# Optimization experiments

Hardware: AMD Instinct MI355X
Metric: run time of the kernel (lower is better)

The kernel has to match this reference:

```python
import jax, jax.numpy as jnp
import numpy as np

BATCH = 16384
N_IN = 128
N_FEAT = N_IN + N_IN * (N_IN + 1) // 2  # 8384
N_OUT = 512


def setup_inputs() -> dict:
    key = jax.random.key(0)
    k1, k2 = jax.random.split(key)
    x = jax.random.normal(k1, (BATCH, N_IN), dtype=jnp.float32)
    # xavier_uniform_ on (in_features, out_features)
    limit = float(np.sqrt(6.0 / (N_FEAT + N_OUT)))
    weight = jax.random.uniform(k2, (N_FEAT, N_OUT), dtype=jnp.float32, minval=-limit, maxval=limit)
    bias = jnp.zeros((N_OUT,), dtype=jnp.float32)
    return {"x": x, "weight": weight, "bias": bias}


def _quadratic_expand(x):
    # Upper-triangle (i<=j) pairwise products in row-major order,
    # matching the torch nested loop (ih, ih+jh).
    n = x.shape[1]
    iu, ju = jnp.triu_indices(n)
    cross = x[:, iu] * x[:, ju]  # [B, n(n+1)/2]
    return jnp.concatenate([x, cross], axis=1)  # [B, n + n(n+1)/2]


def reference(x, weight, bias):
    xc = _quadratic_expand(x)
    return jnp.matmul(xc, weight) + bias
```

## Files before the change

kernel.cpp:

```cpp
#include <hip/hip_runtime.h>

#define NIN    128
#define NOUT   512
#define NBATCH 16384
#define KF     8384
#define KP2    8832
#define NG     (KP2 / 8)
#define NTK2   (KP2 / 64)
#define XSP    136
#define NTK    (KF / 64)
#define XP     136
#define AP     72

typedef float f32x4 __attribute__((ext_vector_type(4)));
typedef _Float16 f16x8 __attribute__((ext_vector_type(8)));
typedef _Float16 f16x4 __attribute__((ext_vector_type(4)));
typedef __bf16 bf16x8 __attribute__((ext_vector_type(8)));
typedef unsigned int u32x4 __attribute__((ext_vector_type(4)));

__device__ __forceinline__ int triS(int i) { return (i * (257 - i)) >> 1; }

__global__ void k_tbl(unsigned int* __restrict__ tbl)
{
  int g = blockIdx.x * 256 + threadIdx.x;
  if (g >= NG) return;
  unsigned int e;
  if (g < 16) {
    e = 135u | ((unsigned)(g * 8) << 16);
  } else {
    int gp = g - 16;
    int b = 0;
    #pragma unroll
    for (int bb = 1; bb <= 15; ++bb) {
      int C = 8 * (16 * bb - bb * (bb - 1) / 2);
      if (gp >= C) b = bb;
    }
    int C   = 8 * (16 * b - b * (b - 1) / 2);
    int r   = gp - C;
    int per = 16 - b;
    int i   = 8 * b + r / per;
    int q   = r % per;
    e = (unsigned)i | ((unsigned)(8 * b + 8 * q) << 16);
  }
  tbl[g] = e;
}

__global__ void k_wt2(const float* __restrict__ W,
                      const unsigned int* __restrict__ tbl,
                      _Float16* __restrict__ Wt)
{
  __shared__ _Float16 tile[64][65];
  const int kb   = blockIdx.x >> 3;
  const int nbw  = blockIdx.x & 7;
  const int lane = threadIdx.x & 63;
  const int grp  = threadIdx.x >> 6;
  #pragma unroll 4
  for (int it = 0; it < 16; ++it) {
    int kl = it * 4 + grp;
    int kp = kb * 64 + kl;
    unsigned int e = tbl[kp >> 3];
    int i = (int)(e & 0xFFFFu);
    int j = (int)(e >> 16) + (kp & 7);
    float v = 0.f;
    if (i == 135) {
      v = W[(size_t)kp * NOUT + nbw * 64 + lane];
    } else if (j >= i) {
      int src = 128 + i * 128 - i * (i - 1) / 2 + (j - i);
      v = W[(size_t)src * NOUT + nbw * 64 + lane];
    }
    tile[kl][lane] = (_Float16)v;
  }
  __syncthreads();
  #pragma unroll 4
  for (int it = 0; it < 16; ++it) {
    int nl = it * 4 + grp;
    Wt[(size_t)(nbw * 64 + nl) * KP2 + kb * 64 + lane] = tile[lane][nl];
  }
}

__global__ __launch_bounds__(256, 2) void k_gemm8(
    const float* __restrict__ X,
    const _Float16* __restrict__ Wt,
    const float* __restrict__ bias,
    const unsigned int* __restrict__ tbl,
    float* __restrict__ out)
{
  __shared__ __align__(16) _Float16 xS[128 * XSP];
  __shared__ __align__(16) _Float16 Bt[2][128 * 64];
  __shared__ unsigned short tbl_s[NG];

  const int tid  = threadIdx.x;
  const int lane = tid & 63;
  const int wid  = tid >> 6;
  const int wm   = wid & 1;
  const int wk   = wid >> 1;
  const int mb   = blockIdx.x >> 2;
  const int nb   = blockIdx.x & 3;

  for (int g = tid; g < NG; g += 256) {
    unsigned int e = tbl[g];
    tbl_s[g] = (unsigned short)((e & 0xFFu) | ((e >> 16) << 8));
  }

  {
    const float* xg = X + (size_t)mb * 128 * NIN;
    const int m = tid >> 1, h = tid & 1;
    #pragma unroll
    for (int it = 0; it < 16; ++it) {
      int c4 = h * 64 + it * 4;
      f32x4 v = *reinterpret_cast<const f32x4*>(xg + m * NIN + c4);
      f16x4 b;
      #pragma unroll
      for (int e2 = 0; e2 < 4; ++e2) b[e2] = (_Float16)v[e2];
      *reinterpret_cast<f16x4*>(&xS[m * XSP + c4]) = b;
    }
    if (tid < 128) xS[tid * XSP + 135] = (_Float16)1.0f;
  }

  const int sn = tid >> 3;
  const int sc = tid & 7;
  const _Float16* wrow = Wt + (size_t)(nb * 128 + sn) * KP2 + sc * 8;
  f16x8 pf[8];

  f32x4 acc[4][8];
  #pragma unroll
  for (int a = 0; a < 4; ++a)
    #pragma unroll
    for (int b = 0; b < 8; ++b)
      acc[a][b] = f32x4{0.f, 0.f, 0.f, 0.f};

  #pragma unroll
  for (int r = 0; r < 8; ++r) {
    int t = r >> 2, rep = r & 3;
    pf[r] = *reinterpret_cast<const f16x8*>(wrow + (size_t)rep * 32 * KP2 + t * 64);
  }
  #pragma unroll
  for (int r = 0; r < 8; ++r) {
    int t = r >> 2, rep = r & 3;
    int n = sn + rep * 32;
    *reinterpret_cast<f16x8*>(&Bt[t][n * 64 + ((sc ^ (n & 7)) * 8)]) = pf[r];
  }
  __syncthreads();

  const int NP = NTK2 / 2;
  for (int p = 0; p < NP; ++p) {
    const int kt = 2 * p + wk;
    if (p + 1 < NP) {
      #pragma unroll
      for (int r = 0; r < 8; ++r) {
        int t = r >> 2, rep = r & 3;
        pf[r] = *reinterpret_cast<const f16x8*>(
            wrow + (size_t)rep * 32 * KP2 + (size_t)(2 * (p + 1) + t) * 64);
      }
    }

    #pragma unroll
    for (int kh = 0; kh < 2; ++kh) {
      unsigned short e = tbl_s[kt * 8 + kh * 4 + (lane >> 4)];
      const int i  = (int)(e & 0xFFu);
      const int j0 = (int)(e >> 8);
      f16x8 af[4];
      #pragma unroll
      for (int mi = 0; mi < 4; ++mi) {
        int m = wm * 64 + mi * 16 + (lane & 15);
        f16x8 va = *reinterpret_cast<const f16x8*>(&xS[m * XSP + j0]);
        _Float16 sv = xS[m * XSP + i];
        f16x8 sv8 = {sv, sv, sv, sv, sv, sv, sv, sv};
        af[mi] = va * sv8;
      }
      const int cb = kh * 4 + (lane >> 4);
      #pragma unroll
      for (int ni = 0; ni < 8; ++ni) {
        int n = ni * 16 + (lane & 15);
        f16x8 bv = *reinterpret_cast<const f16x8*>(
            &Bt[wk][n * 64 + ((cb ^ (n & 7)) * 8)]);
        #pragma unroll
        for (int mi = 0; mi < 4; ++mi)
          acc[mi][ni] = __builtin_amdgcn_mfma_f32_16x16x32_f16(af[mi], bv, acc[mi][ni], 0, 0, 0);
      }
    }

    __syncthreads();
    if (p + 1 < NP) {
      #pragma unroll
      for (int r = 0; r < 8; ++r) {
        int t = r >> 2, rep = r & 3;
        int n = sn + rep * 32;
        *reinterpret_cast<f16x8*>(&Bt[t][n * 64 + ((sc ^ (n & 7)) * 8)]) = pf[r];
      }
      __syncthreads();
    }
  }

  {
    float* myreg = (wid < 2 ? reinterpret_cast<float*>(&Bt[0][0])
                            : reinterpret_cast<float*>(&xS[0])) + (wid & 1) * 4096;
    if (wk == 0) {
      #pragma unroll
      for (int mi = 0; mi < 4; ++mi)
        #pragma unroll
        for (int nj = 0; nj < 4; ++nj)
          *reinterpret_cast<f32x4*>(myreg + ((mi * 4 + nj) * 64 + lane) * 4) = acc[mi][4 + nj];
    } else {
      #pragma unroll
      for (int mi = 0; mi < 4; ++mi)
        #pragma unroll
        for (int nj = 0; nj < 4; ++nj)
          *reinterpret_cast<f32x4*>(myreg + ((mi * 4 + nj) * 64 + lane) * 4) = acc[mi][nj];
    }
    __syncthreads();
    const int pw = wid ^ 2;
    const float* preg = (pw < 2 ? reinterpret_cast<const float*>(&Bt[0][0])
                                : reinterpret_cast<const float*>(&xS[0])) + (pw & 1) * 4096;
    if (wk == 0) {
      #pragma unroll
      for (int nj = 0; nj < 4; ++nj) {
        int n = nb * 128 + nj * 16 + (lane & 15);
        float bv = bias[n];
        #pragma unroll
        for (int mi = 0; mi < 4; ++mi) {
          f32x4 o = *reinterpret_cast<const f32x4*>(preg + ((mi * 4 + nj) * 64 + lane) * 4);
          int mloc = wm * 64 + mi * 16 + ((lane >> 4) << 2);
          #pragma unroll
          for (int q = 0; q < 4; ++q) {
            size_t row = (size_t)mb * 128 + mloc + q;
            out[row * NOUT + n] = acc[mi][nj][q] + o[q] + bv;
          }
        }
      }
    } else {
      #pragma unroll
      for (int nj = 0; nj < 4; ++nj) {
        int n = nb * 128 + (4 + nj) * 16 + (lane & 15);
        float bv = bias[n];
        #pragma unroll
        for (int mi = 0; mi < 4; ++mi) {
          f32x4 o = *reinterpret_cast<const f32x4*>(preg + ((mi * 4 + nj) * 64 + lane) * 4);
          int mloc = wm * 64 + mi * 16 + ((lane >> 4) << 2);
          #pragma unroll
          for (int q = 0; q < 4; ++q) {
            size_t row = (size_t)mb * 128 + mloc + q;
            out[row * NOUT + n] = acc[mi][4 + nj][q] + o[q] + bv;
          }
        }
      }
    }
  }
}

__global__ void k_wt(const float* __restrict__ W, __bf16* __restrict__ Wt)
{
  __shared__ __bf16 tile[64][65];
  const int kb   = blockIdx.x >> 3;
  const int nbw  = blockIdx.x & 7;
  const int lane = threadIdx.x & 63;
  const int grp  = threadIdx.x >> 6;
  #pragma unroll 4
  for (int it = 0; it < 16; ++it) {
    int kl = it * 4 + grp;
    tile[kl][lane] = (__bf16)W[(size_t)(kb * 64 + kl) * NOUT + nbw * 64 + lane];
  }
  __syncthreads();
  #pragma unroll 4
  for (int it = 0; it < 16; ++it) {
    int nl = it * 4 + grp;
    Wt[(size_t)(nbw * 64 + nl) * KF + kb * 64 + lane] = tile[lane][nl];
  }
}

template<bool WS>
__global__ __launch_bounds__(256, 2) void k_gemm(
    const float* __restrict__ X, const float* __restrict__ W,
    const __bf16* __restrict__ Wt, const float* __restrict__ bias,
    float* __restrict__ out)
{
  __shared__ __align__(16) __bf16 xT[128 * XP];
  __shared__ __align__(16) __bf16 At[128 * AP];
  __shared__ __align__(16) __bf16 Bt[128 * AP];
  const int tid = threadIdx.x, lane = tid & 63, wid = tid >> 6;
  const int mb = blockIdx.x >> 2, nb = blockIdx.x & 3;
  const int wr = wid >> 1, wc = wid & 1, kk = lane;
  {
    const float* xg = X + (size_t)mb * 128 * 128;
    #pragma unroll
    for (int it = 0; it < 16; ++it) {
      int row = it * 8 + (tid >> 5);
      int c4 = (tid & 31) * 4;
      f32x4 v = *reinterpret_cast<const f32x4*>(xg + row * 128 + c4);
      #pragma unroll
      for (int e = 0; e < 4; ++e) xT[(c4 + e) * XP + row] = (__bf16)v[e];
    }
  }
  f32x4 acc[4][4];
  #pragma unroll
  for (int a = 0; a < 4; ++a)
    #pragma unroll
    for (int b = 0; b < 4; ++b) acc[a][b] = f32x4{0.f, 0.f, 0.f, 0.f};
  __syncthreads();
  for (int kt = 0; kt < NTK; ++kt) {
    if (WS) {
      #pragma unroll
      for (int rep = 0; rep < 4; ++rep) {
        int id = rep * 256 + tid;
        int n = id >> 3, c = id & 7;
        bf16x8 v = *reinterpret_cast<const bf16x8*>(Wt + (size_t)(nb * 128 + n) * KF + kt * 64 + c * 8);
        *reinterpret_cast<bf16x8*>(&Bt[n * AP + c * 8]) = v;
      }
    } else {
      #pragma unroll
      for (int rep = 0; rep < 8; ++rep) {
        int r = rep * 8 + (tid >> 5);
        int cL = (tid & 31) * 4;
        f32x4 wv = *reinterpret_cast<const f32x4*>(W + (size_t)(kt * 64 + r) * NOUT + nb * 128 + cL);
        #pragma unroll
        for (int e = 0; e < 4; ++e) Bt[(cL + e) * AP + r] = (__bf16)wv[e];
      }
    }
    const int k = kt * 64 + kk;
    if (kt >= 2) {
      int idx = k - 128;
      int i = (int)((257.0f - sqrtf((float)(66049 - 8 * idx))) * 0.5f);
      if (i < 0) i = 0;
      if (i > 127) i = 127;
      while (i < 127 && triS(i + 1) <= idx) ++i;
      while (i > 0 && triS(i) > idx) --i;
      int j = i + (idx - triS(i));
      #pragma unroll
      for (int mg = 0; mg < 4; ++mg) {
        int m0 = wid * 32 + mg * 8;
        bf16x8 va = *reinterpret_cast<const bf16x8*>(&xT[i * XP + m0]);
        bf16x8 vb = *reinterpret_cast<const bf16x8*>(&xT[j * XP + m0]);
        #pragma unroll
        for (int q = 0; q < 8; ++q)
          At[(m0 + q) * AP + kk] = (__bf16)((float)va[q] * (float)vb[q]);
      }
    } else {
      #pragma unroll
      for (int mg = 0; mg < 4; ++mg) {
        int m0 = wid * 32 + mg * 8;
        bf16x8 va = *reinterpret_cast<const bf16x8*>(&xT[k * XP + m0]);
        #pragma unroll
        for (int q = 0; q < 8; ++q) At[(m0 + q) * AP + kk] = va[q];
      }
    }
    __syncthreads();
    #pragma unroll
    for (int kh = 0; kh < 2; ++kh) {
      const int koff = kh * 32 + 8 * (lane >> 4);
      bf16x8 af2[4], bfv[4];
      #pragma unroll
      for (int mi = 0; mi < 4; ++mi) {
        int m = wr * 64 + mi * 16 + (lane & 15);
        af2[mi] = *reinterpret_cast<const bf16x8*>(&At[m * AP + koff]);
      }
      #pragma unroll
      for (int ni = 0; ni < 4; ++ni) {
        int n = wc * 64 + ni * 16 + (lane & 15);
        bfv[ni] = *reinterpret_cast<const bf16x8*>(&Bt[n * AP + koff]);
      }
      #pragma unroll
      for (int mi = 0; mi < 4; ++mi)
        #pragma unroll
        for (int ni = 0; ni < 4; ++ni)
          acc[mi][ni] = __builtin_amdgcn_mfma_f32_16x16x32_bf16(af2[mi], bfv[ni], acc[mi][ni], 0, 0, 0);
    }
    __syncthreads();
  }
  #pragma unroll
  for (int ni = 0; ni < 4; ++ni) {
    int n = nb * 128 + wc * 64 + ni * 16 + (lane & 15);
    float bv = bias[n];
    #pragma unroll
    for (int mi = 0; mi < 4; ++mi) {
      int mloc = wr * 64 + mi * 16 + ((lane >> 4) << 2);
      #pragma unroll
      for (int q = 0; q < 4; ++q) {
        size_t row = (size_t)mb * 128 + mloc + q;
        out[row * NOUT + n] = acc[mi][ni][q] + bv;
      }
    }
  }
}

extern "C" void kernel_launch(void* const* d_in, const int* in_sizes, int n_in,
                              void* d_out, int out_size, void* d_ws, size_t ws_size,
                              hipStream_t stream)
{
  const float* X    = (const float*)d_in[0];
  const float* W    = (const float*)d_in[1];
  const float* bias = (const float*)d_in[2];
  float* out        = (float*)d_out;

  const size_t wt2_bytes = (size_t)NOUT * KP2 * 2;
  const size_t need2     = wt2_bytes + (size_t)NG * 4;
  const size_t wt_bytes  = (size_t)NOUT * KF * 2;

  if (d_ws && ws_size >= need2) {
    _Float16* Wt      = (_Float16*)d_ws;
    unsigned int* tbl = (unsigned int*)((char*)d_ws + wt2_bytes);
    k_tbl<<<dim3((NG + 255) / 256), dim3(256), 0, stream>>>(tbl);
    k_wt2<<<dim3(NTK2 * 8), dim3(256), 0, stream>>>(W, tbl, Wt);
    k_gemm8<<<dim3((NBATCH / 128) * 4), dim3(256), 0, stream>>>(X, Wt, bias, tbl, out);
  } else if (d_ws && ws_size >= wt_bytes) {
    __bf16* Wtb = (__bf16*)d_ws;
    k_wt<<<dim3(NTK * 8), dim3(256), 0, stream>>>(W, Wtb);
    k_gemm<true><<<dim3((NBATCH / 128) * 4), dim3(256), 0, stream>>>(X, W, Wtb, bias, out);
  } else {
    k_gemm<false><<<dim3((NBATCH / 128) * 4), dim3(256), 0, stream>>>(X, W, nullptr, bias, out);
  }
}
```

Baseline: 163.5 us.

## Pre-swizzle weights into MFMA fragment order and load B operands directly to registers

The weight transpose kernel now writes fp16 weights in the exact per-lane MFMA B-fragment layout, so the GEMM kernel reads B fragments straight from global memory into registers and prefetches the next k-tile. This drops the shared-memory B tiles and the two per-iteration block barriers. The separate table kernel is removed and entries are computed inline, and the epilogue reduction is reworked to share one exchange buffer. The cost is that B reuse across waves now comes from cache instead of LDS, with more global load traffic per wave, and the kernel depends on global load latency being hidden by register prefetch.

```diff
diff --git a/kernel.cpp b/kernel.cpp
--- a/kernel.cpp
+++ b/kernel.cpp
@@ -7,6 +7,7 @@
 #define KP2    8832
 #define NG     (KP2 / 8)
 #define NTK2   (KP2 / 64)
+#define NPAIR  (NTK2 / 2)
 #define XSP    136
 #define NTK    (KF / 64)
 #define XP     136
@@ -16,49 +17,40 @@
 typedef _Float16 f16x8 __attribute__((ext_vector_type(8)));
 typedef _Float16 f16x4 __attribute__((ext_vector_type(4)));
 typedef __bf16 bf16x8 __attribute__((ext_vector_type(8)));
-typedef unsigned int u32x4 __attribute__((ext_vector_type(4)));
 
 __device__ __forceinline__ int triS(int i) { return (i * (257 - i)) >> 1; }
 
-__global__ void k_tbl(unsigned int* __restrict__ tbl)
-{
-  int g = blockIdx.x * 256 + threadIdx.x;
-  if (g >= NG) return;
-  unsigned int e;
-  if (g < 16) {
-    e = 135u | ((unsigned)(g * 8) << 16);
-  } else {
-    int gp = g - 16;
-    int b = 0;
-    #pragma unroll
-    for (int bb = 1; bb <= 15; ++bb) {
-      int C = 8 * (16 * bb - bb * (bb - 1) / 2);
-      if (gp >= C) b = bb;
-    }
-    int C   = 8 * (16 * b - b * (b - 1) / 2);
-    int r   = gp - C;
-    int per = 16 - b;
-    int i   = 8 * b + r / per;
-    int q   = r % per;
-    e = (unsigned)i | ((unsigned)(8 * b + 8 * q) << 16);
-  }
-  tbl[g] = e;
-}
-
-__global__ void k_wt2(const float* __restrict__ W,
-                      const unsigned int* __restrict__ tbl,
-                      _Float16* __restrict__ Wt)
+__device__ __forceinline__ unsigned int tbl_entry(int g)
+{
+  if (g < 16) return 135u | ((unsigned)(g * 8) << 16);
+  int gp = g - 16;
+  int b = 0;
+  #pragma unroll
+  for (int bb = 1; bb <= 15; ++bb) {
+    int C = 8 * (16 * bb - bb * (bb - 1) / 2);
+    if (gp >= C) b = bb;
+  }
+  int C   = 8 * (16 * b - b * (b - 1) / 2);
+  int r   = gp - C;
+  int per = 16 - b;
+  int i   = 8 * b + r / per;
+  int q   = r % per;
+  return (unsigned)i | ((unsigned)(8 * b + 8 * q) << 16);
+}
+
+__global__ void k_wtf(const float* __restrict__ W, _Float16* __restrict__ Wtf)
 {
   __shared__ _Float16 tile[64][65];
   const int kb   = blockIdx.x >> 3;
   const int nbw  = blockIdx.x & 7;
-  const int lane = threadIdx.x & 63;
-  const int grp  = threadIdx.x >> 6;
+  const int tid  = threadIdx.x;
+  const int lane = tid & 63;
+  const int grp  = tid >> 6;
   #pragma unroll 4
   for (int it = 0; it < 16; ++it) {
     int kl = it * 4 + grp;
     int kp = kb * 64 + kl;
-    unsigned int e = tbl[kp >> 3];
+    unsigned int e = tbl_entry(kp >> 3);
     int i = (int)(e & 0xFFFFu);
     int j = (int)(e >> 16) + (kp & 7);
     float v = 0.f;
@@ -71,22 +63,28 @@
     tile[kl][lane] = (_Float16)v;
   }
   __syncthreads();
-  #pragma unroll 4
-  for (int it = 0; it < 16; ++it) {
-    int nl = it * 4 + grp;
-    Wt[(size_t)(nbw * 64 + nl) * KP2 + kb * 64 + lane] = tile[lane][nl];
-  }
-}
-
-__global__ __launch_bounds__(256, 2) void k_gemm8(
+  #pragma unroll
+  for (int it = 0; it < 2; ++it) {
+    int c  = it * 256 + tid;
+    int nl = c >> 3;
+    int kc = c & 7;
+    int n  = nbw * 64 + nl;
+    f16x8 v;
+    #pragma unroll
+    for (int e2 = 0; e2 < 8; ++e2) v[e2] = tile[kc * 8 + e2][nl];
+    size_t idx = ((size_t)((n >> 7) * 138 + kb) * 16 + ((kc >> 2) * 8 + ((n >> 4) & 7))) * 64
+               + ((kc & 3) * 16 + (n & 15));
+    *reinterpret_cast<f16x8*>(Wtf + idx * 8) = v;
+  }
+}
+
+__global__ __launch_bounds__(256, 2) void k_gemmA(
     const float* __restrict__ X,
-    const _Float16* __restrict__ Wt,
+    const _Float16* __restrict__ Wtf,
     const float* __restrict__ bias,
-    const unsigned int* __restrict__ tbl,
     float* __restrict__ out)
 {
   __shared__ __align__(16) _Float16 xS[128 * XSP];
-  __shared__ __align__(16) _Float16 Bt[2][128 * 64];
   __shared__ unsigned short tbl_s[NG];
 
   const int tid  = threadIdx.x;
@@ -98,7 +96,7 @@
   const int nb   = blockIdx.x & 3;
 
   for (int g = tid; g < NG; g += 256) {
-    unsigned int e = tbl[g];
+    unsigned int e = tbl_entry(g);
     tbl_s[g] = (unsigned short)((e & 0xFFu) | ((e >> 16) << 8));
   }
 
@@ -116,11 +114,9 @@
     }
     if (tid < 128) xS[tid * XSP + 135] = (_Float16)1.0f;
   }
-
-  const int sn = tid >> 3;
-  const int sc = tid & 7;
-  const _Float16* wrow = Wt + (size_t)(nb * 128 + sn) * KP2 + sc * 8;
-  f16x8 pf[8];
+  __syncthreads();
+
+  const _Float16* wbase = Wtf + (((size_t)(nb * 138) * 16) * 64 + lane) * 8;
 
   f32x4 acc[4][8];
   #pragma unroll
@@ -129,150 +125,101 @@
     for (int b = 0; b < 8; ++b)
       acc[a][b] = f32x4{0.f, 0.f, 0.f, 0.f};
 
-  #pragma unroll
-  for (int r = 0; r < 8; ++r) {
-    int t = r >> 2, rep = r & 3;
-    pf[r] = *reinterpret_cast<const f16x8*>(wrow + (size_t)rep * 32 * KP2 + t * 64);
-  }
-  #pragma unroll
-  for (int r = 0; r < 8; ++r) {
-    int t = r >> 2, rep = r & 3;
-    int n = sn + rep * 32;
-    *reinterpret_cast<f16x8*>(&Bt[t][n * 64 + ((sc ^ (n & 7)) * 8)]) = pf[r];
-  }
-  __syncthreads();
-
-  const int NP = NTK2 / 2;
-  for (int p = 0; p < NP; ++p) {
+  f16x8 bf[2][8];
+  #pragma unroll
+  for (int kh = 0; kh < 2; ++kh)
+    #pragma unroll
+    for (int ni = 0; ni < 8; ++ni)
+      bf[kh][ni] = *reinterpret_cast<const f16x8*>(
+          wbase + ((size_t)wk * 16 + kh * 8 + ni) * 512);
+
+  for (int p = 0; p < NPAIR; ++p) {
     const int kt = 2 * p + wk;
-    if (p + 1 < NP) {
-      #pragma unroll
-      for (int r = 0; r < 8; ++r) {
-        int t = r >> 2, rep = r & 3;
-        pf[r] = *reinterpret_cast<const f16x8*>(
-            wrow + (size_t)rep * 32 * KP2 + (size_t)(2 * (p + 1) + t) * 64);
-      }
-    }
-
     #pragma unroll
     for (int kh = 0; kh < 2; ++kh) {
       unsigned short e = tbl_s[kt * 8 + kh * 4 + (lane >> 4)];
       const int i  = (int)(e & 0xFFu);
       const int j0 = (int)(e >> 8);
-      f16x8 af[4];
       #pragma unroll
       for (int mi = 0; mi < 4; ++mi) {
         int m = wm * 64 + mi * 16 + (lane & 15);
         f16x8 va = *reinterpret_cast<const f16x8*>(&xS[m * XSP + j0]);
         _Float16 sv = xS[m * XSP + i];
         f16x8 sv8 = {sv, sv, sv, sv, sv, sv, sv, sv};
-        af[mi] = va * sv8;
-      }
-      const int cb = kh * 4 + (lane >> 4);
-      #pragma unroll
-      for (int ni = 0; ni < 8; ++ni) {
-        int n = ni * 16 + (lane & 15);
-        f16x8 bv = *reinterpret_cast<const f16x8*>(
-            &Bt[wk][n * 64 + ((cb ^ (n & 7)) * 8)]);
-        #pragma unroll
-        for (int mi = 0; mi < 4; ++mi)
-          acc[mi][ni] = __builtin_amdgcn_mfma_f32_16x16x32_f16(af[mi], bv, acc[mi][ni], 0, 0, 0);
-      }
-    }
-
-    __syncthreads();
-    if (p + 1 < NP) {
-      #pragma unroll
-      for (int r = 0; r < 8; ++r) {
-        int t = r >> 2, rep = r & 3;
-        int n = sn + rep * 32;
-        *reinterpret_cast<f16x8*>(&Bt[t][n * 64 + ((sc ^ (n & 7)) * 8)]) = pf[r];
-      }
-      __syncthreads();
+        f16x8 af = va * sv8;
+        #pragma unroll
+        for (int ni = 0; ni < 8; ++ni)
+          acc[mi][ni] = __builtin_amdgcn_mfma_f32_16x16x32_f16(
+              af, bf[kh][ni], acc[mi][ni], 0, 0, 0);
+      }
+      if (p + 1 < NPAIR) {
+        #pragma unroll
+        for (int ni = 0; ni < 8; ++ni)
+          bf[kh][ni] = *reinterpret_cast<const f16x8*>(
+              wbase + ((size_t)(kt + 2) * 16 + kh * 8 + ni) * 512);
+      }
     }
   }
 
   {
-    float* myreg = (wid < 2 ? reinterpret_cast<float*>(&Bt[0][0])
-                            : reinterpret_cast<float*>(&xS[0])) + (wid & 1) * 4096;
+    float* exch = reinterpret_cast<float*>(&xS[0]) + wm * 4096;
+    const int nbase = nb * 128;
+    const int mbase = mb * 128 + wm * 64;
+
+    __syncthreads();
+    if (wk == 1) {
+      #pragma unroll
+      for (int mi = 0; mi < 4; ++mi)
+        #pragma unroll
+        for (int nj = 0; nj < 4; ++nj)
+          *reinterpret_cast<f32x4*>(exch + ((mi * 4 + nj) * 64 + lane) * 4) = acc[mi][nj];
+    }
+    __syncthreads();
     if (wk == 0) {
       #pragma unroll
+      for (int nj = 0; nj < 4; ++nj) {
+        int n = nbase + nj * 16 + (lane & 15);
+        float bv = bias[n];
+        #pragma unroll
+        for (int mi = 0; mi < 4; ++mi) {
+          f32x4 o = *reinterpret_cast<const f32x4*>(exch + ((mi * 4 + nj) * 64 + lane) * 4);
+          int mloc = mbase + mi * 16 + ((lane >> 4) << 2);
+          #pragma unroll
+          for (int q = 0; q < 4; ++q)
+            out[(size_t)(mloc + q) * NOUT + n] = acc[mi][nj][q] + o[q] + bv;
+        }
+      }
+    }
+    __syncthreads();
+    if (wk == 0) {
+      #pragma unroll
       for (int mi = 0; mi < 4; ++mi)
         #pragma unroll
         for (int nj = 0; nj < 4; ++nj)
-          *reinterpret_cast<f32x4*>(myreg + ((mi * 4 + nj) * 64 + lane) * 4) = acc[mi][4 + nj];
-    } else {
-      #pragma unroll
-      for (int mi = 0; mi < 4; ++mi)
-        #pragma unroll
-        for (int nj = 0; nj < 4; ++nj)
-          *reinterpret_cast<f32x4*>(myreg + ((mi * 4 + nj) * 64 + lane) * 4) = acc[mi][nj];
-    }
-    __syncthreads();
-    const int pw = wid ^ 2;
-    const float* preg = (pw < 2 ? reinterpret_cast<const float*>(&Bt[0][0])
-                                : reinterpret_cast<const float*>(&xS[0])) + (pw & 1) * 4096;
-    if (wk == 0) {
+          *reinterpret_cast<f32x4*>(exch + ((mi * 4 + nj) * 64 + lane) * 4) = acc[mi][4 + nj];
+    }
+    __syncthreads();
+    if (wk == 1) {
       #pragma unroll
       for (int nj = 0; nj < 4; ++nj) {
-        int n = nb * 128 + nj * 16 + (lane & 15);
+        int n = nbase + (4 + nj) * 16 + (lane & 15);
         float bv = bias[n];
         #pragma unroll
         for (int mi = 0; mi < 4; ++mi) {
-          f32x4 o = *reinterpret_cast<const f32x4*>(preg + ((mi * 4 + nj) * 64 + lane) * 4);
-          int mloc = wm * 64 + mi * 16 + ((lane >> 4) << 2);
+          f32x4 o = *reinterpret_cast<const f32x4*>(exch + ((mi * 4 + nj) * 64 + lane) * 4);
+          int mloc = mbase + mi * 16 + ((lane >> 4) << 2);
           #pragma unroll
-          for (int q = 0; q < 4; ++q) {
-            size_t row = (size_t)mb * 128 + mloc + q;
-            out[row * NOUT + n] = acc[mi][nj][q] + o[q] + bv;
-          }
+          for (int q = 0; q < 4; ++q)
+            out[(size_t)(mloc + q) * NOUT + n] = acc[mi][4 + nj][q] + o[q] + bv;
         }
       }
-    } else {
-      #pragma unroll
-      for (int nj = 0; nj < 4; ++nj) {
-        int n = nb * 128 + (4 + nj) * 16 + (lane & 15);
-        float bv = bias[n];
-        #pragma unroll
-        for (int mi = 0; mi < 4; ++mi) {
-          f32x4 o = *reinterpret_cast<const f32x4*>(preg + ((mi * 4 + nj) * 64 + lane) * 4);
-          int mloc = wm * 64 + mi * 16 + ((lane >> 4) << 2);
-          #pragma unroll
-          for (int q = 0; q < 4; ++q) {
-            size_t row = (size_t)mb * 128 + mloc + q;
-            out[row * NOUT + n] = acc[mi][4 + nj][q] + o[q] + bv;
-          }
-        }
-      }
-    }
-  }
-}
-
-__global__ void k_wt(const float* __restrict__ W, __bf16* __restrict__ Wt)
-{
-  __shared__ __bf16 tile[64][65];
-  const int kb   = blockIdx.x >> 3;
-  const int nbw  = blockIdx.x & 7;
-  const int lane = threadIdx.x & 63;
-  const int grp  = threadIdx.x >> 6;
-  #pragma unroll 4
-  for (int it = 0; it < 16; ++it) {
-    int kl = it * 4 + grp;
-    tile[kl][lane] = (__bf16)W[(size_t)(kb * 64 + kl) * NOUT + nbw * 64 + lane];
-  }
-  __syncthreads();
-  #pragma unroll 4
-  for (int it = 0; it < 16; ++it) {
-    int nl = it * 4 + grp;
-    Wt[(size_t)(nbw * 64 + nl) * KF + kb * 64 + lane] = tile[lane][nl];
-  }
-}
-
-template<bool WS>
-__global__ __launch_bounds__(256, 2) void k_gemm(
+    }
+  }
+}
+
+__global__ __launch_bounds__(256, 2) void k_gemm_nws(
     const float* __restrict__ X, const float* __restrict__ W,
-    const __bf16* __restrict__ Wt, const float* __restrict__ bias,
-    float* __restrict__ out)
+    const float* __restrict__ bias, float* __restrict__ out)
 {
   __shared__ __align__(16) __bf16 xT[128 * XP];
   __shared__ __align__(16) __bf16 At[128 * AP];
@@ -298,23 +245,13 @@
     for (int b = 0; b < 4; ++b) acc[a][b] = f32x4{0.f, 0.f, 0.f, 0.f};
   __syncthreads();
   for (int kt = 0; kt < NTK; ++kt) {
-    if (WS) {
-      #pragma unroll
-      for (int rep = 0; rep < 4; ++rep) {
-        int id = rep * 256 + tid;
-        int n = id >> 3, c = id & 7;
-        bf16x8 v = *reinterpret_cast<const bf16x8*>(Wt + (size_t)(nb * 128 + n) * KF + kt * 64 + c * 8);
-        *reinterpret_cast<bf16x8*>(&Bt[n * AP + c * 8]) = v;
-      }
-    } else {
-      #pragma unroll
-      for (int rep = 0; rep < 8; ++rep) {
-        int r = rep * 8 + (tid >> 5);
-        int cL = (tid & 31) * 4;
-        f32x4 wv = *reinterpret_cast<const f32x4*>(W + (size_t)(kt * 64 + r) * NOUT + nb * 128 + cL);
-        #pragma unroll
-        for (int e = 0; e < 4; ++e) Bt[(cL + e) * AP + r] = (__bf16)wv[e];
-      }
+    #pragma unroll
+    for (int rep = 0; rep < 8; ++rep) {
+      int r = rep * 8 + (tid >> 5);
+      int cL = (tid & 31) * 4;
+      f32x4 wv = *reinterpret_cast<const f32x4*>(W + (size_t)(kt * 64 + r) * NOUT + nb * 128 + cL);
+      #pragma unroll
+      for (int e = 0; e < 4; ++e) Bt[(cL + e) * AP + r] = (__bf16)wv[e];
     }
     const int k = kt * 64 + kk;
     if (kt >= 2) {
@@ -391,21 +328,13 @@
   const float* bias = (const float*)d_in[2];
   float* out        = (float*)d_out;
 
-  const size_t wt2_bytes = (size_t)NOUT * KP2 * 2;
-  const size_t need2     = wt2_bytes + (size_t)NG * 4;
-  const size_t wt_bytes  = (size_t)NOUT * KF * 2;
-
-  if (d_ws && ws_size >= need2) {
-    _Float16* Wt      = (_Float16*)d_ws;
-    unsigned int* tbl = (unsigned int*)((char*)d_ws + wt2_bytes);
-    k_tbl<<<dim3((NG + 255) / 256), dim3(256), 0, stream>>>(tbl);
-    k_wt2<<<dim3(NTK2 * 8), dim3(256), 0, stream>>>(W, tbl, Wt);
-    k_gemm8<<<dim3((NBATCH / 128) * 4), dim3(256), 0, stream>>>(X, Wt, bias, tbl, out);
-  } else if (d_ws && ws_size >= wt_bytes) {
-    __bf16* Wtb = (__bf16*)d_ws;
-    k_wt<<<dim3(NTK * 8), dim3(256), 0, stream>>>(W, Wtb);
-    k_gemm<true><<<dim3((NBATCH / 128) * 4), dim3(256), 0, stream>>>(X, W, Wtb, bias, out);
+  const size_t wt_bytes = (size_t)NOUT * KP2 * 2;
+
+  if (d_ws && ws_size >= wt_bytes) {
+    _Float16* Wb = (_Float16*)d_ws;
+    k_wtf<<<dim3(NTK2 * 8), dim3(256), 0, stream>>>(W, Wb);
+    k_gemmA<<<dim3((NBATCH / 128) * 4), dim3(256), 0, stream>>>(X, Wb, bias, out);
   } else {
-    k_gemm<false><<<dim3((NBATCH / 128) * 4), dim3(256), 0, stream>>>(X, W, nullptr, bias, out);
-  }
-}
+    k_gemm_nws<<<dim3((NBATCH / 128) * 4), dim3(256), 0, stream>>>(X, W, bias, out);
+  }
+}
```

Measured after the change: 151.2 us. -7.5%, faster.
